# Kernel optimization log

Measured on AMD Instinct MI355X. Metric: run time of the kernel, lower is better.

## Reference

```python
import jax, jax.numpy as jnp
import numpy as np

B, S, HOPS, DIM, NREL = 1024, 32, 2, 64, 237
NENT, NEDGE = 14541, 272115
SIGMA = 0.1
CFMW = 64


def setup_inputs() -> dict:
    key = jax.random.key(0)
    ks = jax.random.split(key, 20)

    def g(k, shape):
        return (jax.random.normal(k, shape, dtype=jnp.float32) / np.float32(np.sqrt(shape[0])))

    inp = {
        "entity_pairs": jax.random.randint(ks[0], (B, 2), 0, NENT),
        "train_edges": jax.random.randint(ks[1], (B,), 0, NEDGE),
        "labels": jax.random.randint(ks[2], (B,), 0, NREL),
        "entity2edges": jax.random.randint(ks[3], (NENT + 1, S), 0, NEDGE + 1),
        "edge2entities": jax.random.randint(ks[4], (NEDGE + 1, 1), 0, NENT + 1),
        "edge2relation": jax.random.randint(ks[5], (NEDGE + 1,), 0, NREL + 1),
        "t": jax.random.uniform(ks[6], (B,), dtype=jnp.float32),
        "eps": jax.random.normal(ks[7], (B, NREL), dtype=jnp.float32),
        "rel_feat": g(ks[8], (NREL, DIM)),
        "W_agg0": g(ks[9], (DIM, DIM)), "b_agg0": jnp.zeros((DIM,), jnp.float32),
        "W_agg1": g(ks[10], (DIM, NREL)), "b_agg1": jnp.zeros((NREL,), jnp.float32),
        "W_out": g(ks[11], (2 * NREL, NREL)), "b_out": jnp.zeros((NREL,), jnp.float32),
        "mW1": g(ks[12], (NREL + 1, CFMW)), "mb1": jnp.zeros((CFMW,), jnp.float32),
        "mW2": g(ks[13], (CFMW, CFMW)), "mb2": jnp.zeros((CFMW,), jnp.float32),
        "mW3": g(ks[14], (CFMW, CFMW)), "mb3": jnp.zeros((CFMW,), jnp.float32),
        "mW4": g(ks[15], (CFMW, NREL)), "mb4": jnp.zeros((NREL,), jnp.float32),
    }
    return inp


def _side(ent, labels, train_edges, entity2edges, edge2entities, edge2relation, relf, aggs):
    # multi-hop neighbor edge gather + masks (exclude the training edge itself)
    edges_list = [labels]  # hop-0 "edges" are the relation labels
    masks = []
    for i in range(HOPS):
        if i == 0:
            ne = ent.reshape(B, 1)  # (B, 1) source entities
        else:
            ne = edge2entities[edges_list[-1].reshape(-1)].reshape(B, -1)
        nedges = entity2edges[ne.reshape(-1)].reshape(B, -1)  # (B, S**(i+1))
        edges_list.append(nedges)
        masks.append((nedges != train_edges[:, None]).astype(relf.dtype))
    # edge -> relation -> feature
    ev = [relf[edges_list[0]]]  # (B, DIM)
    for edges in edges_list[1:]:
        ev.append(relf[edge2relation[edges]])  # (B, S**h, DIM)
    # iterative mean aggregation (PathCon-style, one entity per edge)
    for i in range(HOPS):
        W, b, act, self_inc = aggs[i]
        d = W.shape[0]
        nxt = []
        for hop in range(HOPS - i):
            neigh = ev[hop + 1].reshape(B, -1, 1, S, d)
            m = masks[hop].reshape(B, -1, 1, S, 1)
            out = jnp.mean(jnp.mean(neigh * m, axis=-2), axis=-2)  # (B, S**hop, d)
            if self_inc:
                out = out + ev[hop].reshape(B, -1, d)
            nxt.append(act(out @ W + b))
        ev = nxt
    return ev[0].reshape(B, NREL)


def reference(entity_pairs, train_edges, labels, entity2edges, edge2entities,
              edge2relation, t, eps, rel_feat, W_agg0, b_agg0, W_agg1, b_agg1,
              W_out, b_out, mW1, mb1, mW2, mb2, mW3, mb3, mW4, mb4):
    relf = jnp.concatenate([rel_feat, jnp.zeros((1, DIM), rel_feat.dtype)], axis=0)
    aggs = [
        (W_agg0, b_agg0, jax.nn.relu, True),    # intermediate hop: relu, self-included
        (W_agg1, b_agg1, lambda x: x, False),   # last hop: identity, no self
    ]
    x0 = _side(entity_pairs[:, 0], labels, train_edges, entity2edges,
               edge2entities, edge2relation, relf, aggs)
    x1 = _side(entity_pairs[:, 1], labels, train_edges, entity2edges,
               edge2entities, edge2relation, relf, aggs)
    output = jnp.concatenate([x0, x1], axis=-1) @ W_out + b_out  # (B, NREL)
    # CFM: xt = (1-t) x0 + t x1 + sigma*eps ; ut = x1 - x0
    tb = t[:, None]
    xt = (1.0 - tb) * x0 + tb * x1 + SIGMA * eps
    h = jnp.concatenate([xt, tb], axis=-1)
    h = jax.nn.selu(h @ mW1 + mb1)
    h = jax.nn.selu(h @ mW2 + mb2)
    h = jax.nn.selu(h @ mW3 + mb3)
    vt = h @ mW4 + mb4
    scores = output * vt
    return scores
```

## Files before the change

### kernel.cpp

```cpp
#include <hip/hip_runtime.h>
#include <math.h>

#define BB 1024
#define S 32
#define DIM 64
#define NREL 237
#define NENT 14541
#define SIGMA 0.1f

#define OFS_WR    0
#define N_WR      (238*64)
#define OFS_WC0   15232
#define N_WC      (64*237)
#define OFS_WC1   (OFS_WC0 + N_WC)
#define OFS_BC    (OFS_WC1 + N_WC)
#define OFS_HC    (OFS_BC + 237)
#define OFS_A     45872

#define LDS_BYTES 18688

__device__ __forceinline__ float selu_f(float x) {
    const float alpha = 1.6732632423543772f;
    const float scale = 1.0507009873554805f;
    return scale * (x > 0.f ? x : alpha * expm1f(x));
}

__global__ __launch_bounds__(256) void pre_wr_kernel(
    const float* __restrict__ rel_feat, const float* __restrict__ W0,
    float* __restrict__ ws) {
    int idx = blockIdx.x * 256 + threadIdx.x;
    if (idx < 238 * 64) {
        int r = idx >> 6, o = idx & 63;
        float acc = 0.f;
        if (r < NREL) {
#pragma unroll 8
            for (int d = 0; d < 64; ++d)
                acc += rel_feat[r * 64 + d] * W0[d * 64 + o];
        }
        ws[OFS_WR + idx] = acc;
    }
}

__global__ __launch_bounds__(512) void mid_kernel(
    const int* __restrict__ e2e_tab, const int* __restrict__ e2r,
    const float* __restrict__ W1, const float* __restrict__ b1,
    const float* __restrict__ W_out, const float* __restrict__ b_out,
    const float* __restrict__ mW1, const float* __restrict__ mb1,
    float* __restrict__ ws) {
    __shared__ int   s_r[1024];
    __shared__ float red[512];
    int blk = blockIdx.x;
    const int tid = threadIdx.x;

    if (blk < 455) {
        const int grp = tid >> 4, c = tid & 15;
        const int ent = blk * 32 + grp;
        const bool ok = ent < (NENT + 1);
        if (ok) {
            int ea = e2e_tab[ent * S + c];
            int eb = e2e_tab[ent * S + 16 + c];
            s_r[grp * 32 + c] = e2r[ea];
            s_r[grp * 32 + 16 + c] = e2r[eb];
        }
        __syncthreads();
        if (ok) {
            const float4* Wr4 = (const float4*)(ws + OFS_WR);
            const int* rr = &s_r[grp * 32];
            float4 acc = make_float4(0.f, 0.f, 0.f, 0.f);
#pragma unroll
            for (int s = 0; s < 32; ++s) {
                float4 v = Wr4[rr[s] * 16 + c];
                acc.x += v.x; acc.y += v.y; acc.z += v.z; acc.w += v.w;
            }
            ((float4*)(ws + OFS_A))[ent * 16 + c] = acc;
        }
        return;
    }
    blk -= 455;
    if (blk < 512) {
        int half = blk >> 8;
        int lb = blk & 255;
        int o = lb >> 2, ct = lb & 3;
        int cl = tid & 63, q = tid >> 6;
        int c = ct * 64 + cl;
        const float* Wsrc = W_out + half * 237 * 237;
        float acc = 0.f;
        if (c < NREL) {
            int k0 = q * 30, k1 = (q == 7) ? 237 : (k0 + 30);
#pragma unroll 4
            for (int k = k0; k < k1; ++k)
                acc += W1[o * 237 + k] * Wsrc[k * 237 + c];
        }
        red[tid] = acc;
        __syncthreads();
        if (q == 0 && c < NREL) {
            float s = 0.f;
#pragma unroll
            for (int qq = 0; qq < 8; ++qq) s += red[qq * 64 + cl];
            ws[(half ? OFS_WC1 : OFS_WC0) + o * 237 + c] = s;
        }
        return;
    }
    blk -= 512;
    if (blk < 4) {
        int cl = tid & 63, q = tid >> 6;
        int c = blk * 64 + cl;
        float acc = 0.f;
        if (c < NREL) {
            int k0 = q * 30, k1 = (q == 7) ? 237 : (k0 + 30);
#pragma unroll 4
            for (int k = k0; k < k1; ++k)
                acc += b1[k] * (W_out[k * 237 + c] + W_out[(237 + k) * 237 + c]);
        }
        red[tid] = acc;
        __syncthreads();
        if (q == 0 && c < NREL) {
            float s = b_out[c];
#pragma unroll
            for (int qq = 0; qq < 8; ++qq) s += red[qq * 64 + cl];
            ws[OFS_BC + c] = s;
        }
        return;
    }
    {
        int w = tid & 63, q = tid >> 6;
        int k0 = q * 30, k1 = (q == 7) ? 237 : (k0 + 30);
        float acc = 0.f;
#pragma unroll 4
        for (int k = k0; k < k1; ++k)
            acc += b1[k] * mW1[k * 64 + w];
        red[tid] = acc;
        __syncthreads();
        if (q == 0) {
            float s = mb1[w];
#pragma unroll
            for (int qq = 0; qq < 8; ++qq) s += red[qq * 64 + w];
            ws[OFS_HC + w] = s;
        }
    }
}

__global__ __launch_bounds__(512, 8) void gf_kernel(
    const int* __restrict__ ep, const int* __restrict__ te_arr,
    const int* __restrict__ e2e_tab, const int* __restrict__ e2ent,
    const int* __restrict__ e2r, const float* __restrict__ b0,
    const float* __restrict__ t_arr, const float* __restrict__ eps,
    const float* __restrict__ W1, const float* __restrict__ mW1,
    const float* __restrict__ mW2, const float* __restrict__ mb2,
    const float* __restrict__ mW3, const float* __restrict__ mb3,
    const float* __restrict__ mW4, const float* __restrict__ mb4,
    const float* __restrict__ ws, float* __restrict__ out) {
    extern __shared__ float smem[];
    float* s_v1   = smem;
    int*   s_r1   = (int*)(smem + 4352);
    int*   s_ent2 = (int*)(smem + 4416);
    float* s_m1   = smem + 4480;
    float* s_ov   = smem + 4544;

    const int tid = threadIdx.x;
    const int b = blockIdx.x;
    const int grp = tid >> 4;
    const int c = tid & 15;
    const int te = te_arr[b];
    const int rte = e2r[te];
    const float4* Wr4 = (const float4*)(ws + OFS_WR);
    const float4* A4  = (const float4*)(ws + OFS_A);
    const float4 b0v  = ((const float4*)b0)[c];
    const float4 wrte = Wr4[rte * 16 + c];

    if (tid < 64) {
        int u = tid >> 5, s = tid & 31;
        int ent = ep[b * 2 + u];
        int e1 = e2e_tab[ent * S + s];
        s_r1[u * 32 + s] = e2r[e1];
        s_m1[u * 32 + s] = (e1 != te) ? 1.0f : 0.0f;
        s_ent2[u * 32 + s] = e2ent[e1];
    }
    __syncthreads();

    const float inv = 1.0f / 32.0f;
#pragma unroll
    for (int u = 0; u < 2; ++u) {
        const int j = grp;
        const int ent2 = s_ent2[u * 32 + j];
        int e2a = e2e_tab[ent2 * S + c];
        int e2b = e2e_tab[ent2 * S + 16 + c];
        int cnt = (e2a == te) + (e2b == te);
        cnt += __shfl_xor(cnt, 1);
        cnt += __shfl_xor(cnt, 2);
        cnt += __shfl_xor(cnt, 4);
        cnt += __shfl_xor(cnt, 8);
        float4 a4   = A4[ent2 * 16 + c];
        float4 self = Wr4[s_r1[u * 32 + j] * 16 + c];
        float fc = (float)cnt;
        float m = s_m1[u * 32 + j];
        float4 r;
        r.x = fmaxf(self.x + (a4.x - fc * wrte.x) * inv + b0v.x, 0.f) * m;
        r.y = fmaxf(self.y + (a4.y - fc * wrte.y) * inv + b0v.y, 0.f) * m;
        r.z = fmaxf(self.z + (a4.z - fc * wrte.z) * inv + b0v.z, 0.f) * m;
        r.w = fmaxf(self.w + (a4.w - fc * wrte.w) * inv + b0v.w, 0.f) * m;
        *((float4*)&s_v1[(u * 32 + j) * 68 + c * 4]) = r;
    }
    __syncthreads();
    if (tid < 128) {
        int u = tid >> 6, w = tid & 63;
        float sum = 0.f;
#pragma unroll 8
        for (int j = 0; j < 32; ++j) sum += s_v1[(u * 32 + j) * 68 + w];
        s_ov[u * 64 + w] = sum * inv;
    }
    __syncthreads();

    float* s_ymix = smem;
    float* s_outv = smem + 240;
    float* s_red  = smem + 480;
    float* s_h    = smem + 992;
    float* s_omix = smem + 1056;
    float* s_vp   = smem + 1120;
    const float tb = t_arr[b];
    const float* Wc0 = ws + OFS_WC0;
    const float* Wc1 = ws + OFS_WC1;
    const float* bc = ws + OFS_BC;
    const float* hc = ws + OFS_HC;

    if (tid < 64)
        s_omix[tid] = (1.f - tb) * s_ov[tid] + tb * s_ov[64 + tid];
    __syncthreads();

    if (tid < 256) {
        if (tid < NREL) {
            float y = 0.f;
#pragma unroll 4
            for (int d = 0; d < 64; ++d)
                y += s_omix[d] * W1[d * 237 + tid];
            s_ymix[tid] = y;
        }
    } else {
        int cc = tid - 256;
        if (cc < NREL) {
            float a = bc[cc];
#pragma unroll 4
            for (int d = 0; d < 64; ++d)
                a += s_ov[d] * Wc0[d * 237 + cc] + s_ov[64 + d] * Wc1[d * 237 + cc];
            s_outv[cc] = a;
        }
    }
    __syncthreads();

    {
        int w = tid & 63, q = tid >> 6;
        int k0 = q * 30, k1 = (q == 7) ? 237 : (k0 + 30);
        const float* e = eps + b * 237;
        float a = 0.f;
#pragma unroll 4
        for (int k = k0; k < k1; ++k)
            a += (SIGMA * e[k] + s_ymix[k]) * mW1[k * 64 + w];
        s_red[tid] = a;
    }
    __syncthreads();
    if (tid < 64) {
        float h = hc[tid] + tb * mW1[237 * 64 + tid];
#pragma unroll
        for (int q = 0; q < 8; ++q) h += s_red[q * 64 + tid];
        s_h[tid] = selu_f(h);
    }
    __syncthreads();

    {
        int w = tid & 63, q = tid >> 6;
        float a = 0.f;
#pragma unroll
        for (int d = q * 8; d < q * 8 + 8; ++d)
            a += s_h[d] * mW2[d * 64 + w];
        s_red[tid] = a;
    }
    __syncthreads();
    if (tid < 64) {
        float v = mb2[tid];
#pragma unroll
        for (int q = 0; q < 8; ++q) v += s_red[q * 64 + tid];
        s_h[tid] = selu_f(v);
    }
    __syncthreads();

    {
        int w = tid & 63, q = tid >> 6;
        float a = 0.f;
#pragma unroll
        for (int d = q * 8; d < q * 8 + 8; ++d)
            a += s_h[d] * mW3[d * 64 + w];
        s_red[tid] = a;
    }
    __syncthreads();
    if (tid < 64) {
        float v = mb3[tid];
#pragma unroll
        for (int q = 0; q < 8; ++q) v += s_red[q * 64 + tid];
        s_h[tid] = selu_f(v);
    }
    __syncthreads();

    {
        int half = tid >> 8, cc = tid & 255;
        if (cc < NREL) {
            float a = 0.f;
#pragma unroll 4
            for (int w = half * 32; w < half * 32 + 32; ++w)
                a += s_h[w] * mW4[w * 237 + cc];
            s_vp[half * 240 + cc] = a;
        }
    }
    __syncthreads();
    if (tid < NREL)
        out[b * 237 + tid] = s_outv[tid] * (mb4[tid] + s_vp[tid] + s_vp[240 + tid]);
}

extern "C" void kernel_launch(void* const* d_in, const int* in_sizes, int n_in,
                              void* d_out, int out_size, void* d_ws, size_t ws_size,
                              hipStream_t stream) {
    const int* ep       = (const int*)d_in[0];
    const int* te       = (const int*)d_in[1];
    const int* e2e      = (const int*)d_in[3];
    const int* e2ent    = (const int*)d_in[4];
    const int* e2r      = (const int*)d_in[5];
    const float* t      = (const float*)d_in[6];
    const float* eps    = (const float*)d_in[7];
    const float* relf   = (const float*)d_in[8];
    const float* W0     = (const float*)d_in[9];
    const float* b0     = (const float*)d_in[10];
    const float* W1     = (const float*)d_in[11];
    const float* b1     = (const float*)d_in[12];
    const float* W_out  = (const float*)d_in[13];
    const float* b_out  = (const float*)d_in[14];
    const float* mW1    = (const float*)d_in[15];
    const float* mb1    = (const float*)d_in[16];
    const float* mW2    = (const float*)d_in[17];
    const float* mb2    = (const float*)d_in[18];
    const float* mW3    = (const float*)d_in[19];
    const float* mb3    = (const float*)d_in[20];
    const float* mW4    = (const float*)d_in[21];
    const float* mb4    = (const float*)d_in[22];
    float* ws  = (float*)d_ws;
    float* out = (float*)d_out;

    hipLaunchKernelGGL(pre_wr_kernel, dim3(60), dim3(256), 0, stream,
                       relf, W0, ws);
    hipLaunchKernelGGL(mid_kernel, dim3(972), dim3(512), 0, stream,
                       e2e, e2r, W1, b1, W_out, b_out, mW1, mb1, ws);
    hipLaunchKernelGGL(gf_kernel, dim3(BB), dim3(512), LDS_BYTES, stream,
                       ep, te, e2e, e2ent, e2r, b0,
                       t, eps, W1, mW1, mW2, mb2, mW3, mb3, mW4, mb4, ws, out);
}
```

Baseline: 141.8 us.

## Process two batch rows per block in gf_kernel with per-half MLP work

The gather/fusion kernel now handles two batch elements per 512-thread block, launching half as many blocks. The first stage gathers the neighbour edges for four entity sides. In the dense MLP stage each 256-thread half works on its own row, with fewer partial reductions and the ymix/outv projections fused into one loop. This is meant to raise per-thread work and cut idle threads in the serial MLP chain. In exchange it doubles LDS per block, drops the occupancy hint from launch bounds, and launches only 512 blocks, which may under-fill the GPU.

Measured after the change: 143.8 us. Within noise of the previous version (+1.4%).

```diff
diff --git a/kernel.cpp b/kernel.cpp
--- a/kernel.cpp
+++ b/kernel.cpp
@@ -17,7 +17,7 @@
 #define OFS_HC    (OFS_BC + 237)
 #define OFS_A     45872
 
-#define LDS_BYTES 18688
+#define LDS_BYTES 37376
 
 __device__ __forceinline__ float selu_f(float x) {
     const float alpha = 1.6732632423543772f;
@@ -140,7 +140,7 @@
     }
 }
 
-__global__ __launch_bounds__(512, 8) void gf_kernel(
+__global__ __launch_bounds__(512) void gf_kernel(
     const int* __restrict__ ep, const int* __restrict__ te_arr,
     const int* __restrict__ e2e_tab, const int* __restrict__ e2ent,
     const int* __restrict__ e2r, const float* __restrict__ b0,
@@ -152,40 +152,45 @@
     const float* __restrict__ ws, float* __restrict__ out) {
     extern __shared__ float smem[];
     float* s_v1   = smem;
-    int*   s_r1   = (int*)(smem + 4352);
-    int*   s_ent2 = (int*)(smem + 4416);
-    float* s_m1   = smem + 4480;
-    float* s_ov   = smem + 4544;
+    int*   s_r1   = (int*)(smem + 8704);
+    int*   s_ent2 = (int*)(smem + 8832);
+    float* s_m1   = smem + 8960;
+    float* s_ov   = smem + 9088;
 
     const int tid = threadIdx.x;
-    const int b = blockIdx.x;
+    const int bb = blockIdx.x * 2;
     const int grp = tid >> 4;
     const int c = tid & 15;
-    const int te = te_arr[b];
-    const int rte = e2r[te];
+    const int te0 = te_arr[bb];
+    const int te1 = te_arr[bb + 1];
     const float4* Wr4 = (const float4*)(ws + OFS_WR);
     const float4* A4  = (const float4*)(ws + OFS_A);
     const float4 b0v  = ((const float4*)b0)[c];
-    const float4 wrte = Wr4[rte * 16 + c];
-
-    if (tid < 64) {
+    const float4 wrte0 = Wr4[e2r[te0] * 16 + c];
+    const float4 wrte1 = Wr4[e2r[te1] * 16 + c];
+
+    if (tid < 128) {
         int u = tid >> 5, s = tid & 31;
-        int ent = ep[b * 2 + u];
+        int b_ = bb + (u >> 1);
+        int te_u = (u >> 1) ? te1 : te0;
+        int ent = ep[b_ * 2 + (u & 1)];
         int e1 = e2e_tab[ent * S + s];
         s_r1[u * 32 + s] = e2r[e1];
-        s_m1[u * 32 + s] = (e1 != te) ? 1.0f : 0.0f;
+        s_m1[u * 32 + s] = (e1 != te_u) ? 1.0f : 0.0f;
         s_ent2[u * 32 + s] = e2ent[e1];
     }
     __syncthreads();
 
     const float inv = 1.0f / 32.0f;
 #pragma unroll
-    for (int u = 0; u < 2; ++u) {
+    for (int u = 0; u < 4; ++u) {
+        const int te_u = (u >> 1) ? te1 : te0;
+        const float4 wrte = (u >> 1) ? wrte1 : wrte0;
         const int j = grp;
         const int ent2 = s_ent2[u * 32 + j];
         int e2a = e2e_tab[ent2 * S + c];
         int e2b = e2e_tab[ent2 * S + 16 + c];
-        int cnt = (e2a == te) + (e2b == te);
+        int cnt = (e2a == te_u) + (e2b == te_u);
         cnt += __shfl_xor(cnt, 1);
         cnt += __shfl_xor(cnt, 2);
         cnt += __shfl_xor(cnt, 4);
@@ -202,7 +207,7 @@
         *((float4*)&s_v1[(u * 32 + j) * 68 + c * 4]) = r;
     }
     __syncthreads();
-    if (tid < 128) {
+    if (tid < 256) {
         int u = tid >> 6, w = tid & 63;
         float sum = 0.f;
 #pragma unroll 8
@@ -211,108 +216,88 @@
     }
     __syncthreads();
 
-    float* s_ymix = smem;
-    float* s_outv = smem + 240;
-    float* s_red  = smem + 480;
-    float* s_h    = smem + 992;
-    float* s_omix = smem + 1056;
-    float* s_vp   = smem + 1120;
-    const float tb = t_arr[b];
+    const int p  = tid >> 8;
+    const int lt = tid & 255;
+    float* s_ymix = smem + p * 1024;
+    float* s_outv = smem + p * 1024 + 240;
+    float* s_red  = smem + p * 1024 + 480;
+    float* s_h    = smem + p * 1024 + 736;
+    const float tb = t_arr[bb + p];
+    const float* ovp = s_ov + p * 128;
     const float* Wc0 = ws + OFS_WC0;
     const float* Wc1 = ws + OFS_WC1;
     const float* bc = ws + OFS_BC;
     const float* hc = ws + OFS_HC;
 
-    if (tid < 64)
-        s_omix[tid] = (1.f - tb) * s_ov[tid] + tb * s_ov[64 + tid];
-    __syncthreads();
-
-    if (tid < 256) {
-        if (tid < NREL) {
-            float y = 0.f;
-#pragma unroll 4
-            for (int d = 0; d < 64; ++d)
-                y += s_omix[d] * W1[d * 237 + tid];
-            s_ymix[tid] = y;
-        }
-    } else {
-        int cc = tid - 256;
-        if (cc < NREL) {
-            float a = bc[cc];
-#pragma unroll 4
-            for (int d = 0; d < 64; ++d)
-                a += s_ov[d] * Wc0[d * 237 + cc] + s_ov[64 + d] * Wc1[d * 237 + cc];
-            s_outv[cc] = a;
-        }
+    if (lt < NREL) {
+        float y = 0.f, a = bc[lt];
+        const float om = 1.f - tb;
+#pragma unroll 4
+        for (int d = 0; d < 64; ++d) {
+            float o0 = ovp[d], o1 = ovp[64 + d];
+            y += (om * o0 + tb * o1) * W1[d * 237 + lt];
+            a += o0 * Wc0[d * 237 + lt] + o1 * Wc1[d * 237 + lt];
+        }
+        s_ymix[lt] = y;
+        s_outv[lt] = a;
     }
     __syncthreads();
 
     {
-        int w = tid & 63, q = tid >> 6;
-        int k0 = q * 30, k1 = (q == 7) ? 237 : (k0 + 30);
-        const float* e = eps + b * 237;
+        int w = lt & 63, q = lt >> 6;
+        int k0 = q * 60, k1 = (q == 3) ? 237 : (k0 + 60);
+        const float* e = eps + (bb + p) * 237;
         float a = 0.f;
 #pragma unroll 4
         for (int k = k0; k < k1; ++k)
             a += (SIGMA * e[k] + s_ymix[k]) * mW1[k * 64 + w];
-        s_red[tid] = a;
-    }
-    __syncthreads();
-    if (tid < 64) {
-        float h = hc[tid] + tb * mW1[237 * 64 + tid];
-#pragma unroll
-        for (int q = 0; q < 8; ++q) h += s_red[q * 64 + tid];
-        s_h[tid] = selu_f(h);
+        s_red[lt] = a;
+    }
+    __syncthreads();
+    if (lt < 64) {
+        float h = hc[lt] + tb * mW1[237 * 64 + lt]
+                + s_red[lt] + s_red[64 + lt] + s_red[128 + lt] + s_red[192 + lt];
+        s_h[lt] = selu_f(h);
     }
     __syncthreads();
 
     {
-        int w = tid & 63, q = tid >> 6;
+        int w = lt & 63, q = lt >> 6;
         float a = 0.f;
 #pragma unroll
-        for (int d = q * 8; d < q * 8 + 8; ++d)
+        for (int d = q * 16; d < q * 16 + 16; ++d)
             a += s_h[d] * mW2[d * 64 + w];
-        s_red[tid] = a;
-    }
-    __syncthreads();
-    if (tid < 64) {
-        float v = mb2[tid];
-#pragma unroll
-        for (int q = 0; q < 8; ++q) v += s_red[q * 64 + tid];
-        s_h[tid] = selu_f(v);
+        s_red[lt] = a;
+    }
+    __syncthreads();
+    if (lt < 64) {
+        float v = mb2[lt] + s_red[lt] + s_red[64 + lt] + s_red[128 + lt] + s_red[192 + lt];
+        s_h[lt] = selu_f(v);
     }
     __syncthreads();
 
     {
-        int w = tid & 63, q = tid >> 6;
+        int w = lt & 63, q = lt >> 6;
         float a = 0.f;
 #pragma unroll
-        for (int d = q * 8; d < q * 8 + 8; ++d)
+        for (int d = q * 16; d < q * 16 + 16; ++d)
             a += s_h[d] * mW3[d * 64 + w];
-        s_red[tid] = a;
-    }
-    __syncthreads();
-    if (tid < 64) {
-        float v = mb3[tid];
-#pragma unroll
-        for (int q = 0; q < 8; ++q) v += s_red[q * 64 + tid];
-        s_h[tid] = selu_f(v);
-    }
-    __syncthreads();
-
-    {
-        int half = tid >> 8, cc = tid & 255;
-        if (cc < NREL) {
-            float a = 0.f;
-#pragma unroll 4
-            for (int w = half * 32; w < half * 32 + 32; ++w)
-                a += s_h[w] * mW4[w * 237 + cc];
-            s_vp[half * 240 + cc] = a;
-        }
-    }
-    __syncthreads();
-    if (tid < NREL)
-        out[b * 237 + tid] = s_outv[tid] * (mb4[tid] + s_vp[tid] + s_vp[240 + tid]);
+        s_red[lt] = a;
+    }
+    __syncthreads();
+    if (lt < 64) {
+        float v = mb3[lt] + s_red[lt] + s_red[64 + lt] + s_red[128 + lt] + s_red[192 + lt];
+        s_h[lt] = selu_f(v);
+    }
+    __syncthreads();
+
+    if (lt < NREL) {
+        float a = mb4[lt];
+#pragma unroll 4
+        for (int w = 0; w < 64; ++w)
+            a += s_h[w] * mW4[w * 237 + lt];
+        out[(bb + p) * 237 + lt] = s_outv[lt] * a;
+    }
 }
 
 extern "C" void kernel_launch(void* const* d_in, const int* in_sizes, int n_in,
@@ -347,7 +332,7 @@
                        relf, W0, ws);
     hipLaunchKernelGGL(mid_kernel, dim3(972), dim3(512), 0, stream,
                        e2e, e2r, W1, b1, W_out, b_out, mW1, mb1, ws);
-    hipLaunchKernelGGL(gf_kernel, dim3(BB), dim3(512), LDS_BYTES, stream,
+    hipLaunchKernelGGL(gf_kernel, dim3(BB / 2), dim3(512), LDS_BYTES, stream,
                        ep, te, e2e, e2ent, e2r, b0,
                        t, eps, W1, mW1, mW2, mb2, mW3, mb3, mW4, mb4, ws, out);
 }
```
